# Performance work log

Measured on AMD Instinct MI355X. Metric: run time of the kernel, lower is better.

## Reference

```python
import jax, jax.numpy as jnp
import numpy as np

N = 50000          # nodes
E = 1600000        # edges (avg degree 32)
D_IN = 128
D_OUT = 128
NEG_SLOPE = 0.01   # F.leaky_relu default (module ignores its negative_slope attr)


def setup_inputs() -> dict:
    key = jax.random.key(0)
    k = jax.random.split(key, 7)
    h = jax.random.normal(k[0], (N, D_IN), dtype=jnp.float32)
    embedding = jax.random.normal(k[1], (N, D_OUT), dtype=jnp.float32)
    # params (xavier-ish scaling)
    W_lin = jax.random.normal(k[2], (D_OUT, D_IN), dtype=jnp.float32) * (2.0 / (D_IN + D_OUT)) ** 0.5
    w_fc = jax.random.normal(k[3], (1, 2 * D_OUT), dtype=jnp.float32) * (2.0 / (2 * D_OUT + 1)) ** 0.5
    w_emb = jax.random.normal(k[4], (1, 2 * D_OUT), dtype=jnp.float32) * (2.0 / (2 * D_OUT + 1)) ** 0.5
    src = jax.random.randint(k[5], (E,), 0, N, dtype=jnp.int64 if jax.config.jax_enable_x64 else jnp.int32)
    dst = jax.random.randint(k[6], (E,), 0, N, dtype=jnp.int64 if jax.config.jax_enable_x64 else jnp.int32)
    return {"h": h, "embedding": embedding, "W_lin": W_lin, "w_fc": w_fc,
            "w_emb": w_emb, "src": src, "dst": dst}


def reference(h, embedding, W_lin, w_fc, w_emb, src, dst):
    n = h.shape[0]
    d = W_lin.shape[0]
    # z = lin(h): [N, out]
    z = h @ W_lin.T
    # attn_fc(cat(z_src, z_dst)) + attn_embed(cat(e_src, e_dst)) split into per-node
    # scalar scores so we gather [E] scalars instead of materializing [E, 2*out].
    s_fc_src = z @ w_fc[0, :d]            # [N]
    s_fc_dst = z @ w_fc[0, d:]            # [N]
    s_em_src = embedding @ w_emb[0, :d]   # [N]
    s_em_dst = embedding @ w_emb[0, d:]   # [N]
    a = (s_fc_src + s_em_src)[src] + (s_fc_dst + s_em_dst)[dst]   # [E]
    e = jnp.where(a > 0, a, NEG_SLOPE * a)  # leaky_relu, slope 0.01
    # segment softmax over incoming edges of each dst node
    m = jax.ops.segment_max(e, dst, num_segments=n)               # [N]
    e_exp = jnp.exp(e - m[dst])                                   # [E]
    denom = jax.ops.segment_sum(e_exp, dst, num_segments=n)       # [N]
    alpha = e_exp / denom[dst]                                    # [E]
    # weighted neighbor aggregation: h_out[v] = sum_{(u->v)} alpha * z[u]
    h_out = jax.ops.segment_sum(alpha[:, None] * z[src], dst, num_segments=n)
    return h_out
```

## Files before the change

kernel.cpp:

```cpp
#include <hip/hip_runtime.h>
#include <hip/hip_bf16.h>

#define D 128
#define BSH 7
#define BDST 128
#define NCHK 1024
#define CHCAP 1600
#define CAPB 5120
#define SL 8

typedef __attribute__((ext_vector_type(8))) short short8;
typedef __attribute__((ext_vector_type(4))) float f32x4;
typedef __attribute__((ext_vector_type(2))) float f32x2;

__device__ __forceinline__ unsigned short f2bf(float f) {
  unsigned u = __float_as_uint(f);
  unsigned r = (u + 0x7FFFu + ((u >> 16) & 1u)) >> 16;
  return (unsigned short)r;
}

__global__ __launch_bounds__(256) void k_wconv(const float* __restrict__ W,
                                               unsigned short* __restrict__ Wb,
                                               int* __restrict__ bincur, int NB) {
  const int i = blockIdx.x * 256 + threadIdx.x;
  if (i < NB) bincur[i] = 0;
  float4 f = ((const float4*)W)[i];
  ushort4 o;
  o.x = f2bf(f.x); o.y = f2bf(f.y); o.z = f2bf(f.z); o.w = f2bf(f.w);
  ((ushort4*)Wb)[i] = o;
}

__global__ __launch_bounds__(256) void k_combo(
    const float* __restrict__ h, const unsigned short* __restrict__ Wb,
    const float* __restrict__ w_fc, const float* __restrict__ emb,
    const float* __restrict__ w_emb, unsigned* __restrict__ zd,
    float* __restrict__ a_src, float* __restrict__ a_dst,
    const int* __restrict__ src, const int* __restrict__ dst,
    int* __restrict__ bincur, unsigned* __restrict__ binrec,
    int n, int E, int NB, int CHSZ) {
  __shared__ unsigned recbuf[CHCAP];
  __shared__ int hl[512], gbase[512], loff[512], lcur[512];
  __shared__ int sh[256];
  __shared__ float sfs[4][16], sfd[4][16];
  const int tid = threadIdx.x;

  if ((int)blockIdx.x < NCHK) {
    const int c = blockIdx.x;
    const int beg = c * CHSZ, end = min(beg + CHSZ, E);
    const int cnt = end - beg;
    for (int i = tid; i < 512; i += 256) { hl[i] = 0; lcur[i] = 0; }
    __syncthreads();
    for (int i = beg + tid; i < end; i += 256) atomicAdd(&hl[dst[i] >> BSH], 1);
    __syncthreads();
    for (int b = tid; b < NB; b += 256) {
      int cb = hl[b];
      gbase[b] = cb > 0 ? atomicAdd(&bincur[b], cb) : 0;
    }
    int v0 = hl[2 * tid], v1 = hl[2 * tid + 1];
    int s = v0 + v1;
    sh[tid] = s;
    __syncthreads();
    for (int off = 1; off < 256; off <<= 1) {
      int a = (tid >= off) ? sh[tid - off] : 0;
      __syncthreads();
      sh[tid] += a;
      __syncthreads();
    }
    int base = sh[tid] - s;
    loff[2 * tid] = base;
    loff[2 * tid + 1] = base + v0;
    __syncthreads();
    for (int i = beg + tid; i < end; i += 256) {
      int d = dst[i];
      int b = d >> BSH;
      unsigned r = ((unsigned)src[i] << 16) | (unsigned)d;
      int lp = atomicAdd(&lcur[b], 1);
      recbuf[loff[b] + lp] = r;
    }
    __syncthreads();
    for (int i = tid; i < cnt; i += 256) {
      unsigned r = recbuf[i];
      int b = (int)(r & 0xFFFFu) >> BSH;
      binrec[(size_t)b * CAPB + gbase[b] + (i - loff[b])] = r;
    }
    return;
  }

  const int lane = tid & 63;
  const int wid = tid >> 6;
  const int m0 = (blockIdx.x - NCHK) * 64 + wid * 16;
  if (m0 >= n) return;
  const int c = lane & 15;
  const int g = lane >> 4;

  int arow = m0 + c;
  if (arow >= n) arow = n - 1;
  const float4* hrow = (const float4*)(h + (size_t)arow * 128);

  short8 afr[4];
#pragma unroll
  for (int s = 0; s < 4; ++s) {
    float4 f0 = hrow[8 * s + 2 * g];
    float4 f1 = hrow[8 * s + 2 * g + 1];
    short8 a;
    a[0] = (short)f2bf(f0.x); a[1] = (short)f2bf(f0.y);
    a[2] = (short)f2bf(f0.z); a[3] = (short)f2bf(f0.w);
    a[4] = (short)f2bf(f1.x); a[5] = (short)f2bf(f1.y);
    a[6] = (short)f2bf(f1.z); a[7] = (short)f2bf(f1.w);
    afr[s] = a;
  }

  f32x4 acc[8];
#pragma unroll
  for (int t = 0; t < 8; ++t) acc[t] = (f32x4){0.f, 0.f, 0.f, 0.f};

#pragma unroll
  for (int s = 0; s < 4; ++s) {
#pragma unroll
    for (int t = 0; t < 8; ++t) {
      short8 b = *(const short8*)(Wb + ((size_t)(t * 16 + c) * 128 + 32 * s + 8 * g));
      acc[t] = __builtin_amdgcn_mfma_f32_16x16x32_bf16(afr[s], b, acc[t], 0, 0, 0);
    }
  }

  float wfs[8], wfd[8];
#pragma unroll
  for (int t = 0; t < 8; ++t) {
    wfs[t] = w_fc[t * 16 + c];
    wfd[t] = w_fc[128 + t * 16 + c];
  }

  const int rbase = m0 + 4 * g;
#pragma unroll
  for (int r = 0; r < 4; ++r) {
    const int row = rbase + r;
    if (row < n) {
#pragma unroll
      for (int tp = 0; tp < 4; ++tp) {
        unsigned dw = ((unsigned)f2bf(acc[tp + 4][r]) << 16) | (unsigned)f2bf(acc[tp][r]);
        zd[(size_t)row * 64 + tp * 16 + c] = dw;
      }
    }
    float ps = 0.f, pd = 0.f;
#pragma unroll
    for (int t = 0; t < 8; ++t) {
      ps += acc[t][r] * wfs[t];
      pd += acc[t][r] * wfd[t];
    }
#pragma unroll
    for (int off = 1; off < 16; off <<= 1) {
      ps += __shfl_xor(ps, off, 64);
      pd += __shfl_xor(pd, off, 64);
    }
    if (c == 0) {
      sfs[wid][4 * g + r] = ps;
      sfd[wid][4 * g + r] = pd;
    }
  }
  __syncthreads();

  const int nloc = lane >> 2;
  const int qc = lane & 3;
  const int node2 = m0 + nloc;
  float es = 0.f, ed = 0.f;
  if (node2 < n) {
    const float4* er = (const float4*)(emb + (size_t)node2 * 128 + qc * 32);
    const float4* wsp = (const float4*)(w_emb + qc * 32);
    const float4* wdp = (const float4*)(w_emb + 128 + qc * 32);
#pragma unroll
    for (int j = 0; j < 8; ++j) {
      float4 e4 = er[j], s4 = wsp[j], d4 = wdp[j];
      es += e4.x * s4.x + e4.y * s4.y + e4.z * s4.z + e4.w * s4.w;
      ed += e4.x * d4.x + e4.y * d4.y + e4.z * d4.z + e4.w * d4.w;
    }
  }
  es += __shfl_xor(es, 1, 64); es += __shfl_xor(es, 2, 64);
  ed += __shfl_xor(ed, 1, 64); ed += __shfl_xor(ed, 2, 64);
  if (qc == 0 && node2 < n) {
    a_src[node2] = es + sfs[wid][nloc];
    a_dst[node2] = ed + sfd[wid][nloc];
  }
}

__global__ __launch_bounds__(256) void k_build(const unsigned* __restrict__ binrec,
                                               const int* __restrict__ bincur,
                                               const float* __restrict__ a_src,
                                               const float* __restrict__ a_dst,
                                               int2* __restrict__ row2,
                                               int2* __restrict__ csr2, int n) {
  __shared__ int hist[BDST * SL];
  __shared__ int excl[BDST * SL];
  __shared__ int sh[256];
  __shared__ float adl[BDST];
  const int tid = threadIdx.x, b = blockIdx.x;
  const int cntb = bincur[b];
  const unsigned* rb = binrec + (size_t)b * CAPB;
  const int base = b * CAPB;

  for (int k = tid; k < BDST * SL; k += 256) hist[k] = 0;
  if (tid < BDST) {
    int v = b * BDST + tid;
    adl[tid] = (v < n) ? a_dst[v] : 0.f;
  }
  __syncthreads();
  for (int i = tid; i < cntb; i += 256) {
    unsigned r = rb[i];
    int dl = r & (BDST - 1);
    int sv = (int)(r >> 16);
    atomicAdd(&hist[dl * SL + (sv >> 13)], 1);
  }
  __syncthreads();
  const int k0 = tid * 4;
  int v4[4], s = 0;
#pragma unroll
  for (int j = 0; j < 4; ++j) { v4[j] = hist[k0 + j]; s += v4[j]; }
  sh[tid] = s;
  __syncthreads();
  for (int off = 1; off < 256; off <<= 1) {
    int a = (tid >= off) ? sh[tid - off] : 0;
    __syncthreads();
    sh[tid] += a;
    __syncthreads();
  }
  int e0 = sh[tid] - s;
#pragma unroll
  for (int j = 0; j < 4; ++j) { excl[k0 + j] = e0; e0 += v4[j]; }
  __syncthreads();
  if (tid < BDST) {
    int bg = excl[tid * SL];
    int en = (tid == BDST - 1) ? cntb : excl[(tid + 1) * SL];
    int v = b * BDST + tid;
    if (v < n) row2[v] = make_int2(base + bg, base + en);
  }
  __syncthreads();
  for (int i = tid; i < cntb; i += 256) {
    unsigned r = rb[i];
    int dl = r & (BDST - 1);
    int sv = (int)(r >> 16);
    float a = a_src[sv] + adl[dl];
    float e = a > 0.f ? a : 0.01f * a;
    float ew = __expf(e);
    int pos = base + atomicAdd(&excl[dl * SL + (sv >> 13)], 1);
    csr2[pos] = make_int2(sv, __float_as_int(ew));
  }
}

__global__ __launch_bounds__(256) void k_agg(const unsigned* __restrict__ zd,
                                             const int2* __restrict__ row2,
                                             const int2* __restrict__ csr2,
                                             float* __restrict__ out, int n) {
  const int lane = threadIdx.x & 63;
  const int grp = lane >> 4;
  const int sub = lane & 15;
  const int v = blockIdx.x * 4 + (threadIdx.x >> 6);
  if (v >= n) return;
  const int2 be = row2[v];
  const int beg = be.x, end = be.y;

  f32x2 acc2[4];
#pragma unroll
  for (int j = 0; j < 4; ++j) acc2[j] = (f32x2){0.f, 0.f};
  float ews = 0.f;

#pragma unroll 4
  for (int i = beg + grp; i < end; i += 4) {
    const int2 e2 = csr2[i];
    const float ew = __int_as_float(e2.y);
    const uint4 zz = ((const uint4*)zd)[(size_t)e2.x * 16 + sub];
    ews += ew;
    const f32x2 ew2 = {ew, ew};
    f32x2 z0 = {__uint_as_float(zz.x << 16), __uint_as_float(zz.x & 0xffff0000u)};
    f32x2 z1 = {__uint_as_float(zz.y << 16), __uint_as_float(zz.y & 0xffff0000u)};
    f32x2 z2 = {__uint_as_float(zz.z << 16), __uint_as_float(zz.z & 0xffff0000u)};
    f32x2 z3 = {__uint_as_float(zz.w << 16), __uint_as_float(zz.w & 0xffff0000u)};
    acc2[0] += ew2 * z0;
    acc2[1] += ew2 * z1;
    acc2[2] += ew2 * z2;
    acc2[3] += ew2 * z3;
  }

#pragma unroll
  for (int off = 16; off <= 32; off <<= 1) {
    ews += __shfl_xor(ews, off, 64);
#pragma unroll
    for (int j = 0; j < 4; ++j) {
      acc2[j][0] += __shfl_xor(acc2[j][0], off, 64);
      acc2[j][1] += __shfl_xor(acc2[j][1], off, 64);
    }
  }

  if (grp == 0) {
    const float inv = (end > beg) ? 1.f / ews : 0.f;
    float4 olo = make_float4(acc2[0][0] * inv, acc2[1][0] * inv, acc2[2][0] * inv, acc2[3][0] * inv);
    float4 ohi = make_float4(acc2[0][1] * inv, acc2[1][1] * inv, acc2[2][1] * inv, acc2[3][1] * inv);
    ((float4*)out)[(size_t)v * 32 + sub] = olo;
    ((float4*)out)[(size_t)v * 32 + 16 + sub] = ohi;
  }
}

extern "C" void kernel_launch(void* const* d_in, const int* in_sizes, int n_in,
                              void* d_out, int out_size, void* d_ws, size_t ws_size,
                              hipStream_t stream) {
  const float* h = (const float*)d_in[0];
  const float* emb = (const float*)d_in[1];
  const float* W = (const float*)d_in[2];
  const float* wfc = (const float*)d_in[3];
  const float* wemb = (const float*)d_in[4];
  const int* src = (const int*)d_in[5];
  const int* dst = (const int*)d_in[6];
  const int n = in_sizes[0] / D;
  const int E = in_sizes[5];
  const int NB = (n + BDST - 1) >> BSH;
  const int CHSZ = (E + NCHK - 1) / NCHK;
  const int NLIN = (n + 63) / 64;

  char* ws = (char*)d_ws;
  size_t off = 0;
  auto alloc = [&](size_t bytes) {
    void* p = ws + off;
    off = (off + bytes + 255) & ~(size_t)255;
    return p;
  };
  unsigned* zd = (unsigned*)alloc((size_t)n * 64 * 4);
  unsigned short* Wb = (unsigned short*)alloc(D * D * 2);
  float* a_src = (float*)alloc((size_t)n * 4);
  float* a_dst = (float*)alloc((size_t)n * 4);
  int* bincur = (int*)alloc((size_t)NB * 4);
  int2* row2 = (int2*)alloc((size_t)n * 8);
  unsigned* binrec = (unsigned*)alloc((size_t)NB * CAPB * 4);
  int2* csr2 = (int2*)alloc((size_t)NB * CAPB * 8);
  (void)off;
  (void)ws_size;

  k_wconv<<<(D * D / 4 + 255) / 256, 256, 0, stream>>>(W, Wb, bincur, NB);
  k_combo<<<NCHK + NLIN, 256, 0, stream>>>(h, Wb, wfc, emb, wemb, zd, a_src, a_dst,
                                           src, dst, bincur, binrec, n, E, NB, CHSZ);
  k_build<<<NB, 256, 0, stream>>>(binrec, bincur, a_src, a_dst, row2, csr2, n);
  k_agg<<<(n + 3) / 4, 256, 0, stream>>>(zd, row2, csr2, (float*)d_out, n);
}
```

Baseline: 140.5 us.

## Drop source-slice sub-bucketing in CSR build and halve chunk count

The CSR build kernel no longer sub-sorts each destination's edges into eight source-index slices. It uses a plain per-destination histogram and a 128-entry scan, which shrinks the shared-memory histogram and the scan work. The chunk constants also change (fewer, larger chunks) for the binning pass. The cost is that edges within a row are no longer grouped by source range, so gathers of z rows in the aggregation kernel may lose cache locality.

```diff
diff --git a/kernel.cpp b/kernel.cpp
--- a/kernel.cpp
+++ b/kernel.cpp
@@ -4,10 +4,9 @@
 #define D 128
 #define BSH 7
 #define BDST 128
-#define NCHK 1024
-#define CHCAP 1600
+#define NCHK 512
+#define CHCAP 3200
 #define CAPB 5120
-#define SL 8
 
 typedef __attribute__((ext_vector_type(8))) short short8;
 typedef __attribute__((ext_vector_type(4))) float f32x4;
@@ -188,49 +187,36 @@
                                                const float* __restrict__ a_dst,
                                                int2* __restrict__ row2,
                                                int2* __restrict__ csr2, int n) {
-  __shared__ int hist[BDST * SL];
-  __shared__ int excl[BDST * SL];
-  __shared__ int sh[256];
+  __shared__ int hist[BDST], lrow[BDST], cur[BDST];
   __shared__ float adl[BDST];
   const int tid = threadIdx.x, b = blockIdx.x;
   const int cntb = bincur[b];
   const unsigned* rb = binrec + (size_t)b * CAPB;
   const int base = b * CAPB;
 
-  for (int k = tid; k < BDST * SL; k += 256) hist[k] = 0;
   if (tid < BDST) {
+    hist[tid] = 0;
     int v = b * BDST + tid;
     adl[tid] = (v < n) ? a_dst[v] : 0.f;
   }
   __syncthreads();
-  for (int i = tid; i < cntb; i += 256) {
-    unsigned r = rb[i];
-    int dl = r & (BDST - 1);
-    int sv = (int)(r >> 16);
-    atomicAdd(&hist[dl * SL + (sv >> 13)], 1);
-  }
-  __syncthreads();
-  const int k0 = tid * 4;
-  int v4[4], s = 0;
-#pragma unroll
-  for (int j = 0; j < 4; ++j) { v4[j] = hist[k0 + j]; s += v4[j]; }
-  sh[tid] = s;
-  __syncthreads();
-  for (int off = 1; off < 256; off <<= 1) {
-    int a = (tid >= off) ? sh[tid - off] : 0;
-    __syncthreads();
-    sh[tid] += a;
-    __syncthreads();
-  }
-  int e0 = sh[tid] - s;
-#pragma unroll
-  for (int j = 0; j < 4; ++j) { excl[k0 + j] = e0; e0 += v4[j]; }
-  __syncthreads();
+  for (int i = tid; i < cntb; i += 256)
+    atomicAdd(&hist[rb[i] & (BDST - 1)], 1);
+  __syncthreads();
+  if (tid < BDST) lrow[tid] = hist[tid];
+  __syncthreads();
+  for (int off = 1; off < BDST; off <<= 1) {
+    int a = (tid < BDST && tid >= off) ? lrow[tid - off] : 0;
+    __syncthreads();
+    if (tid < BDST) lrow[tid] += a;
+    __syncthreads();
+  }
   if (tid < BDST) {
-    int bg = excl[tid * SL];
-    int en = (tid == BDST - 1) ? cntb : excl[(tid + 1) * SL];
+    int e = lrow[tid];
+    int s = e - hist[tid];
+    cur[tid] = s;
     int v = b * BDST + tid;
-    if (v < n) row2[v] = make_int2(base + bg, base + en);
+    if (v < n) row2[v] = make_int2(base + s, base + e);
   }
   __syncthreads();
   for (int i = tid; i < cntb; i += 256) {
@@ -240,7 +226,7 @@
     float a = a_src[sv] + adl[dl];
     float e = a > 0.f ? a : 0.01f * a;
     float ew = __expf(e);
-    int pos = base + atomicAdd(&excl[dl * SL + (sv >> 13)], 1);
+    int pos = base + atomicAdd(&cur[dl], 1);
     csr2[pos] = make_int2(sv, __float_as_int(ew));
   }
 }
```

Result: faster. 126.6 us (-9.9%).
